# Optimization experiments

Hardware: AMD Instinct MI355X
Metric: run time of the kernel (lower is better)

Reference implementation:

```python
import jax, jax.numpy as jnp
import numpy as np

EARTH_R_MILES = 3958.8
NEG_INF = -1e30  # finite sentinel; exp underflows to 0 exactly

def haversine(lat1, lon1, lat2, lon2):
    lat1, lon1 = jnp.deg2rad(lat1), jnp.deg2rad(lon1)
    lat2, lon2 = jnp.deg2rad(lat2), jnp.deg2rad(lon2)
    dlat = lat2 - lat1
    dlon = lon2 - lon1
    a = jnp.sin(dlat / 2) ** 2 + jnp.cos(lat1) * jnp.cos(lat2) * jnp.sin(dlon / 2) ** 2
    c = 2.0 * jnp.arctan2(jnp.sqrt(a), jnp.sqrt(1.0 - a))
    return EARTH_R_MILES * c

def setup_inputs() -> dict:
    key = jax.random.key(0)
    k1, k2, k3, k4 = jax.random.split(key, 4)
    B, NBINS, M = 8192, 125, 4096
    preds_lonlat = jax.random.normal(k1, (B, 2), dtype=jnp.float32) * 10.0
    # candidate [lon, lat] coords per bin, padded to M
    bin_coords = jax.random.uniform(k2, (NBINS, M, 2), dtype=jnp.float32) * 10.0
    # three categorical columns, each in [0, 5)
    x_vals = jax.random.randint(k3, (B, 3), 0, 5, dtype=jnp.int64)
    # ragged bin sizes in [1, M] (non-empty; original skips empty bins)
    bin_counts = jax.random.randint(k4, (NBINS,), 1, M + 1, dtype=jnp.int64)
    return {"preds_lonlat": preds_lonlat, "bin_coords": bin_coords,
            "x_vals": x_vals, "bin_counts": bin_counts}

def reference(preds_lonlat, bin_coords, x_vals, bin_counts):
    tau = 0.25
    M = bin_coords.shape[1]
    # flat bin id from categorical key (5 categories per column)
    bin_ids = x_vals[:, 0] * 25 + x_vals[:, 1] * 5 + x_vals[:, 2]      # [B]
    cand = bin_coords[bin_ids]                                          # [B, M, 2] (lon, lat)
    counts = bin_counts[bin_ids]                                        # [B]
    mask = jnp.arange(M)[None, :] < counts[:, None]                     # [B, M]
    lon_p = preds_lonlat[:, 0:1]                                        # [B, 1]
    lat_p = preds_lonlat[:, 1:2]
    dists = haversine(lat_p, lon_p, cand[..., 1], cand[..., 0])         # [B, M]
    logits = jnp.where(mask, -dists / tau, NEG_INF)
    soft_min = -tau * jax.scipy.special.logsumexp(logits, axis=1)       # [B]
    valid = counts > 0
    n_valid = jnp.maximum(jnp.sum(valid), 1)
    loss = jnp.sum(jnp.where(valid, soft_min, 0.0)) / n_valid
    return loss
```

## Files before the change

### kernel.cpp

```cpp
#include <hip/hip_runtime.h>
#include <math.h>

#define D2R      0.017453292519943295f
#define TWO_R    7917.6f
#define RPI2     12435.698f
#define TAU_LN2  0.17328679513998632f
#define K_EXP2   5.770780163555854f
#define MBIG     1.0e30f
#define DMASK    2.0e30f
#define NBINS    125
#define P        8
#define CH       1024
#define MAXCH    4
#define NG_MAX   1152

__device__ __forceinline__ float fexp2(float x) { return __builtin_amdgcn_exp2f(x); }
__device__ __forceinline__ float rfl(float x) {
  return __int_as_float(__builtin_amdgcn_readfirstlane(__float_as_int(x)));
}

#define W_ACCF(w)   ((float*)(w))
#define W_ACCI(w)   ((int*)((char*)(w) + 4))
#define W_NG(w)     ((int*)((char*)(w) + 8))
#define W_HIST(w)   ((int*)((char*)(w) + 16))
#define W_CUR(w)    ((int*)((char*)(w) + 528))
#define W_PBASE(w)  ((int*)((char*)(w) + 1040))
#define W_WREC(w)   ((int4*)((char*)(w) + 1552))
#define W_PTRIG(w)  ((float4*)((char*)(w) + 19984))
#define W_PM(w)     ((float*)((char*)(w) + 151056))
#define W_PS(w)     ((float*)((char*)(w) + 298512))

__global__ __launch_bounds__(256) void g1_hist(
    const int* __restrict__ xv, void* __restrict__ w, int B) {
  int i = blockIdx.x * 256 + threadIdx.x;
  if (i < B) {
    int bin = xv[3 * i] * 25 + xv[3 * i + 1] * 5 + xv[3 * i + 2];
    atomicAdd(&W_HIST(w)[bin], 1);
  }
}

__global__ __launch_bounds__(128) void g2_scan(
    const int* __restrict__ bin_counts, void* __restrict__ w) {
  __shared__ int h[NBINS], cc[NBINS], pb[NBINS], gb[NBINS];
  const int t = threadIdx.x;
  if (t < NBINS) { h[t] = W_HIST(w)[t]; cc[t] = bin_counts[t]; }
  __syncthreads();
  if (t == 0) {
    int base = 0, g = 0;
    for (int b = 0; b < NBINS; ++b) {
      pb[b] = base; base += h[b];
      gb[b] = g;    g += (h[b] + P - 1) / P;
    }
    *W_NG(w) = g;
  }
  __syncthreads();
  if (t < NBINS) {
    W_PBASE(w)[t] = pb[t];
    int ng = (h[t] + P - 1) / P, g0 = gb[t], cnt = cc[t];
    for (int g = 0; g < ng; ++g) {
      int pbp = (pb[t] + g * P) | (min(P, h[t] - g * P) << 20);
      W_WREC(w)[g0 + g] = make_int4(t, pbp, cnt, g);
    }
  }
}

__global__ __launch_bounds__(256) void g3_scatter(
    const float2* __restrict__ preds, const int* __restrict__ xv,
    void* __restrict__ w, int B) {
  int i = blockIdx.x * 256 + threadIdx.x;
  if (i < B) {
    int bin = xv[3 * i] * 25 + xv[3 * i + 1] * 5 + xv[3 * i + 2];
    int pos = W_PBASE(w)[bin] + atomicAdd(&W_CUR(w)[bin], 1);
    float2 p = preds[i];
    float sA, cA, sO, cO;
    __sincosf(p.y * D2R, &sA, &cA);
    __sincosf(p.x * D2R, &sO, &cO);
    W_PTRIG(w)[pos] = make_float4(cA, sA, cO, sO);
  }
}

__global__ __launch_bounds__(256) void lse_main(
    const float2* __restrict__ bc, void* __restrict__ w, int M) {
  const int gi = blockIdx.x >> 2;
  if (gi >= *W_NG(w)) return;
  const int c = blockIdx.x & 3;

  const int4 rec = W_WREC(w)[gi];
  const int bin = rec.x, cnt = rec.z;
  const int nch = (cnt + CH - 1) >> 10;
  if (c >= nch) return;
  const int pb = rec.y & 0xFFFFF;
  const int tid = threadIdx.x;

  const float4* __restrict__ ptrig = W_PTRIG(w);
  const int pcm1 = (rec.y >> 20) - 1;
  float cA[P], sA[P], cO[P], sO[P];
#pragma unroll
  for (int p = 0; p < P; ++p) {
    float4 t = ptrig[pb + min(p, pcm1)];
    cA[p] = rfl(t.x); sA[p] = rfl(t.y); cO[p] = rfl(t.z); sO[p] = rfl(t.w);
  }

  const float2* __restrict__ cb = bc + (size_t)bin * (size_t)M;
  const int c0 = c << 10;
  const int cend = min(cnt, c0 + CH);
  const int nst = (cend - c0 + 255) >> 8;

  float m[P], s[P];
#pragma unroll
  for (int p = 0; p < P; ++p) { m[p] = MBIG; s[p] = 0.0f; }

  float2 cur = cb[min(c0 + tid, cend - 1)];
  for (int st = 0; st < nst; ++st) {
    const int idx = c0 + (st << 8) + tid;
    float2 nxt = cb[min(idx + 256, cend - 1)];
    float sla, cla, slo, clo;
    __sincosf(cur.y * D2R, &sla, &cla);
    __sincosf(cur.x * D2R, &slo, &clo);
    const bool valid = idx < cend;
#pragma unroll
    for (int p = 0; p < P; ++p) {
      float pp    = cA[p] * cla;
      float cdlat = fmaf(sA[p], sla, pp);
      float cdlon = fmaf(cO[p], clo, sO[p] * slo);
      float t1 = fmaf(-0.5f, cdlat, 0.5f);
      float t2 = fmaf(-0.5f, cdlon, 0.5f);
      float a  = fminf(fmaxf(fmaf(pp, t2, t1), 0.0f), 1.0f);
      float x  = sqrtf(a);
      float pl = fmaf(x, -0.0012624911f, 0.0066700901f);
      pl = fmaf(x, pl, -0.0170881256f);
      pl = fmaf(x, pl,  0.0308918810f);
      pl = fmaf(x, pl, -0.0501743046f);
      pl = fmaf(x, pl,  0.0889789874f);
      pl = fmaf(x, pl, -0.2145988016f);
      pl = fmaf(x, pl,  1.5707963050f);
      float wq = sqrtf(1.0f - x);
      float d  = fmaf(-TWO_R, wq * pl, RPI2);
      d = valid ? d : DMASK;
      float mn = fminf(m[p], d);
      s[p] = fmaf(s[p], fexp2((mn - m[p]) * K_EXP2), fexp2((mn - d) * K_EXP2));
      m[p] = mn;
    }
    cur = nxt;
  }

#pragma unroll
  for (int p = 0; p < P; ++p) {
    float mw = m[p];
#pragma unroll
    for (int o = 32; o; o >>= 1) mw = fminf(mw, __shfl_xor(mw, o));
    float sp = s[p] * fexp2((mw - m[p]) * K_EXP2);
#pragma unroll
    for (int o = 32; o; o >>= 1) sp += __shfl_xor(sp, o);
    m[p] = mw; s[p] = sp;
  }

  __shared__ float redm[4][P], reds[4][P];
  const int wave = tid >> 6;
  if ((tid & 63) == 0) {
#pragma unroll
    for (int p = 0; p < P; ++p) { redm[wave][p] = m[p]; reds[wave][p] = s[p]; }
  }
  __syncthreads();
  if (tid < P) {
    float M4 = fminf(fminf(redm[0][tid], redm[1][tid]),
                     fminf(redm[2][tid], redm[3][tid]));
    float S4 = reds[0][tid] * fexp2((M4 - redm[0][tid]) * K_EXP2)
             + reds[1][tid] * fexp2((M4 - redm[1][tid]) * K_EXP2)
             + reds[2][tid] * fexp2((M4 - redm[2][tid]) * K_EXP2)
             + reds[3][tid] * fexp2((M4 - redm[3][tid]) * K_EXP2);
    W_PM(w)[gi * 32 + (c << 3) + tid] = M4;
    W_PS(w)[gi * 32 + (c << 3) + tid] = S4;
  }
}

__global__ __launch_bounds__(64) void merge_kernel(void* __restrict__ w) {
  const int gi = blockIdx.x;
  if (gi >= *W_NG(w)) return;
  const int4 rec = W_WREC(w)[gi];
  const int cnt = rec.z;
  if (cnt <= 0) return;
  const int nch = (cnt + CH - 1) >> 10;
  const int pcount = rec.y >> 20;
  const int p = threadIdx.x;

  float soft = 0.0f;
  if (p < P) {
    float m = W_PM(w)[gi * 32 + p];
    float s = W_PS(w)[gi * 32 + p];
    for (int c = 1; c < nch; ++c) {
      float mo = W_PM(w)[gi * 32 + (c << 3) + p];
      float so = W_PS(w)[gi * 32 + (c << 3) + p];
      float mn = fminf(m, mo);
      s = fmaf(s, fexp2((mn - m) * K_EXP2), so * fexp2((mn - mo) * K_EXP2));
      m = mn;
    }
    float val = m - TAU_LN2 * __log2f(s);
    soft = (p < pcount) ? val : 0.0f;
  }
#pragma unroll
  for (int o = 32; o; o >>= 1) soft += __shfl_xor(soft, o);
  if (p == 0) {
    atomicAdd(W_ACCF(w), soft);
    atomicAdd(W_ACCI(w), pcount);
  }
}

__global__ void fin_kernel(const void* __restrict__ w, float* __restrict__ out) {
  int nv = *W_ACCI((void*)w);
  if (nv < 1) nv = 1;
  out[0] = *W_ACCF((void*)w) / (float)nv;
}

extern "C" void kernel_launch(void* const* d_in, const int* in_sizes, int n_in,
                              void* d_out, int out_size, void* d_ws, size_t ws_size,
                              hipStream_t stream) {
  const float2* preds      = (const float2*)d_in[0];
  const float2* bin_coords = (const float2*)d_in[1];
  const int*    x_vals     = (const int*)d_in[2];
  const int*    bin_counts = (const int*)d_in[3];
  float*        out        = (float*)d_out;

  const int B = in_sizes[0] / 2;
  const int M = (in_sizes[1] / 2) / NBINS;

  hipMemsetAsync(d_ws, 0, 1040, stream);

  const int pblk = (B + 255) / 256;
  g1_hist<<<pblk, 256, 0, stream>>>(x_vals, d_ws, B);
  g2_scan<<<1, 128, 0, stream>>>(bin_counts, d_ws);
  g3_scatter<<<pblk, 256, 0, stream>>>(preds, x_vals, d_ws, B);

  lse_main<<<NG_MAX * MAXCH, 256, 0, stream>>>(bin_coords, d_ws, M);

  merge_kernel<<<NG_MAX, 64, 0, stream>>>(d_ws);
  fin_kernel<<<1, 1, 0, stream>>>(d_ws, out);
}
```

Baseline: 167.9 us.

## Fuse grouping into one block and merge work into persistent main kernel

```diff
diff --git a/kernel.cpp b/kernel.cpp
--- a/kernel.cpp
+++ b/kernel.cpp
@@ -2,75 +2,76 @@
 #include <math.h>
 
 #define D2R      0.017453292519943295f
-#define TWO_R    7917.6f
-#define RPI2     12435.698f
 #define TAU_LN2  0.17328679513998632f
-#define K_EXP2   5.770780163555854f
+#define KR       45690.73f
+#define KRP      71763.68f
 #define MBIG     1.0e30f
 #define DMASK    2.0e30f
 #define NBINS    125
 #define P        8
 #define CH       1024
-#define MAXCH    4
 #define NG_MAX   1152
+#define NBLK     1024
 
 __device__ __forceinline__ float fexp2(float x) { return __builtin_amdgcn_exp2f(x); }
 __device__ __forceinline__ float rfl(float x) {
   return __int_as_float(__builtin_amdgcn_readfirstlane(__float_as_int(x)));
 }
 
-#define W_ACCF(w)   ((float*)(w))
-#define W_ACCI(w)   ((int*)((char*)(w) + 4))
-#define W_NG(w)     ((int*)((char*)(w) + 8))
-#define W_HIST(w)   ((int*)((char*)(w) + 16))
-#define W_CUR(w)    ((int*)((char*)(w) + 528))
-#define W_PBASE(w)  ((int*)((char*)(w) + 1040))
-#define W_WREC(w)   ((int4*)((char*)(w) + 1552))
-#define W_PTRIG(w)  ((float4*)((char*)(w) + 19984))
-#define W_PM(w)     ((float*)((char*)(w) + 151056))
-#define W_PS(w)     ((float*)((char*)(w) + 298512))
-
-__global__ __launch_bounds__(256) void g1_hist(
-    const int* __restrict__ xv, void* __restrict__ w, int B) {
-  int i = blockIdx.x * 256 + threadIdx.x;
-  if (i < B) {
+#define W_NI(w)    ((int*)(w))
+#define W_NGR(w)   ((int*)((char*)(w) + 4))
+#define W_DONE(w)  ((int*)((char*)(w) + 8))
+#define W_GREC(w)  ((int2*)((char*)(w) + 16))
+#define W_IREC(w)  ((int4*)((char*)(w) + 9232))
+#define W_PTRIG(w) ((float4*)((char*)(w) + 82960))
+#define W_PM(w)    ((float*)((char*)(w) + 214032))
+#define W_PS(w)    ((float*)((char*)(w) + 361488))
+
+__global__ __launch_bounds__(1024) void group_kernel(
+    const float2* __restrict__ preds, const int* __restrict__ xv,
+    const int* __restrict__ bin_counts, void* __restrict__ w, int B) {
+  __shared__ int h[NBINS], cur[NBINS], pb[NBINS], gb[NBINS], ib[NBINS], cc[NBINS];
+  const int tid = threadIdx.x;
+
+  if (tid < NBINS) { h[tid] = 0; cc[tid] = bin_counts[tid]; }
+  __syncthreads();
+
+  for (int i = tid; i < B; i += 1024) {
     int bin = xv[3 * i] * 25 + xv[3 * i + 1] * 5 + xv[3 * i + 2];
-    atomicAdd(&W_HIST(w)[bin], 1);
-  }
-}
-
-__global__ __launch_bounds__(128) void g2_scan(
-    const int* __restrict__ bin_counts, void* __restrict__ w) {
-  __shared__ int h[NBINS], cc[NBINS], pb[NBINS], gb[NBINS];
-  const int t = threadIdx.x;
-  if (t < NBINS) { h[t] = W_HIST(w)[t]; cc[t] = bin_counts[t]; }
-  __syncthreads();
-  if (t == 0) {
-    int base = 0, g = 0;
+    atomicAdd(&h[bin], 1);
+  }
+  __syncthreads();
+
+  if (tid == 0) {
+    int base = 0, g = 0, it = 0;
     for (int b = 0; b < NBINS; ++b) {
-      pb[b] = base; base += h[b];
-      gb[b] = g;    g += (h[b] + P - 1) / P;
-    }
-    *W_NG(w) = g;
-  }
-  __syncthreads();
-  if (t < NBINS) {
-    W_PBASE(w)[t] = pb[t];
-    int ng = (h[t] + P - 1) / P, g0 = gb[t], cnt = cc[t];
+      pb[b] = base; gb[b] = g; ib[b] = it;
+      int ngb  = (h[b] + 7) >> 3;
+      int nchb = (cc[b] + CH - 1) >> 10;
+      base += h[b]; g += ngb; it += ngb * nchb;
+    }
+    *W_NI(w) = it; *W_NGR(w) = g; *W_DONE(w) = 0;
+  }
+  __syncthreads();
+
+  if (tid < NBINS) {
+    cur[tid] = 0;
+    const int b = tid, hb = h[b], cb_ = cc[b];
+    const int ng = (hb + 7) >> 3, nch = (cb_ + CH - 1) >> 10;
+    const int g0 = gb[b], i0 = ib[b], p0 = pb[b];
     for (int g = 0; g < ng; ++g) {
-      int pbp = (pb[t] + g * P) | (min(P, h[t] - g * P) << 20);
-      W_WREC(w)[g0 + g] = make_int4(t, pbp, cnt, g);
-    }
-  }
-}
-
-__global__ __launch_bounds__(256) void g3_scatter(
-    const float2* __restrict__ preds, const int* __restrict__ xv,
-    void* __restrict__ w, int B) {
-  int i = blockIdx.x * 256 + threadIdx.x;
-  if (i < B) {
+      int pc = min(P, hb - g * P);
+      W_GREC(w)[g0 + g] = make_int2(pc, cb_);
+      for (int c = 0; c < nch; ++c)
+        W_IREC(w)[i0 + g * nch + c] =
+            make_int4(b, (p0 + g * P) | (pc << 20), cb_, ((g0 + g) << 2) | c);
+    }
+  }
+  __syncthreads();
+
+  for (int i = tid; i < B; i += 1024) {
     int bin = xv[3 * i] * 25 + xv[3 * i + 1] * 5 + xv[3 * i + 2];
-    int pos = W_PBASE(w)[bin] + atomicAdd(&W_CUR(w)[bin], 1);
+    int pos = pb[bin] + atomicAdd(&cur[bin], 1);
     float2 p = preds[i];
     float sA, cA, sO, cO;
     __sincosf(p.y * D2R, &sA, &cA);
@@ -79,137 +80,145 @@
   }
 }
 
-__global__ __launch_bounds__(256) void lse_main(
-    const float2* __restrict__ bc, void* __restrict__ w, int M) {
-  const int gi = blockIdx.x >> 2;
-  if (gi >= *W_NG(w)) return;
-  const int c = blockIdx.x & 3;
-
-  const int4 rec = W_WREC(w)[gi];
-  const int bin = rec.x, cnt = rec.z;
-  const int nch = (cnt + CH - 1) >> 10;
-  if (c >= nch) return;
-  const int pb = rec.y & 0xFFFFF;
-  const int tid = threadIdx.x;
-
-  const float4* __restrict__ ptrig = W_PTRIG(w);
-  const int pcm1 = (rec.y >> 20) - 1;
-  float cA[P], sA[P], cO[P], sO[P];
-#pragma unroll
-  for (int p = 0; p < P; ++p) {
-    float4 t = ptrig[pb + min(p, pcm1)];
-    cA[p] = rfl(t.x); sA[p] = rfl(t.y); cO[p] = rfl(t.z); sO[p] = rfl(t.w);
-  }
-
-  const float2* __restrict__ cb = bc + (size_t)bin * (size_t)M;
-  const int c0 = c << 10;
-  const int cend = min(cnt, c0 + CH);
-  const int nst = (cend - c0 + 255) >> 8;
-
-  float m[P], s[P];
-#pragma unroll
-  for (int p = 0; p < P; ++p) { m[p] = MBIG; s[p] = 0.0f; }
-
-  float2 cur = cb[min(c0 + tid, cend - 1)];
-  for (int st = 0; st < nst; ++st) {
-    const int idx = c0 + (st << 8) + tid;
-    float2 nxt = cb[min(idx + 256, cend - 1)];
-    float sla, cla, slo, clo;
-    __sincosf(cur.y * D2R, &sla, &cla);
-    __sincosf(cur.x * D2R, &slo, &clo);
-    const bool valid = idx < cend;
+__global__ __launch_bounds__(256) void main_kernel(
+    const float2* __restrict__ bc, void* __restrict__ w, int M,
+    float* __restrict__ out) {
+  const int bid = blockIdx.x, tid = threadIdx.x;
+  const int ni = *W_NI(w);
+
+  __shared__ float redm[4][P], reds[4][P];
+  __shared__ int sticket;
+
+  for (int i = bid; i < ni; i += NBLK) {
+    const int4 rec = W_IREC(w)[i];
+    const int bin = rec.x, cnt = rec.z;
+    const int pbb = rec.y & 0xFFFFF, pq = rec.y >> 20;
+    const int gi = rec.w >> 2, c = rec.w & 3;
+
+    float cA[P], sA[P], cO[P], sO[P];
 #pragma unroll
     for (int p = 0; p < P; ++p) {
-      float pp    = cA[p] * cla;
-      float cdlat = fmaf(sA[p], sla, pp);
-      float cdlon = fmaf(cO[p], clo, sO[p] * slo);
-      float t1 = fmaf(-0.5f, cdlat, 0.5f);
-      float t2 = fmaf(-0.5f, cdlon, 0.5f);
-      float a  = fminf(fmaxf(fmaf(pp, t2, t1), 0.0f), 1.0f);
-      float x  = sqrtf(a);
-      float pl = fmaf(x, -0.0012624911f, 0.0066700901f);
-      pl = fmaf(x, pl, -0.0170881256f);
-      pl = fmaf(x, pl,  0.0308918810f);
-      pl = fmaf(x, pl, -0.0501743046f);
-      pl = fmaf(x, pl,  0.0889789874f);
-      pl = fmaf(x, pl, -0.2145988016f);
-      pl = fmaf(x, pl,  1.5707963050f);
-      float wq = sqrtf(1.0f - x);
-      float d  = fmaf(-TWO_R, wq * pl, RPI2);
-      d = valid ? d : DMASK;
-      float mn = fminf(m[p], d);
-      s[p] = fmaf(s[p], fexp2((mn - m[p]) * K_EXP2), fexp2((mn - d) * K_EXP2));
-      m[p] = mn;
-    }
-    cur = nxt;
-  }
-
-#pragma unroll
-  for (int p = 0; p < P; ++p) {
-    float mw = m[p];
-#pragma unroll
-    for (int o = 32; o; o >>= 1) mw = fminf(mw, __shfl_xor(mw, o));
-    float sp = s[p] * fexp2((mw - m[p]) * K_EXP2);
-#pragma unroll
-    for (int o = 32; o; o >>= 1) sp += __shfl_xor(sp, o);
-    m[p] = mw; s[p] = sp;
-  }
-
-  __shared__ float redm[4][P], reds[4][P];
-  const int wave = tid >> 6;
-  if ((tid & 63) == 0) {
-#pragma unroll
-    for (int p = 0; p < P; ++p) { redm[wave][p] = m[p]; reds[wave][p] = s[p]; }
-  }
-  __syncthreads();
-  if (tid < P) {
-    float M4 = fminf(fminf(redm[0][tid], redm[1][tid]),
-                     fminf(redm[2][tid], redm[3][tid]));
-    float S4 = reds[0][tid] * fexp2((M4 - redm[0][tid]) * K_EXP2)
-             + reds[1][tid] * fexp2((M4 - redm[1][tid]) * K_EXP2)
-             + reds[2][tid] * fexp2((M4 - redm[2][tid]) * K_EXP2)
-             + reds[3][tid] * fexp2((M4 - redm[3][tid]) * K_EXP2);
-    W_PM(w)[gi * 32 + (c << 3) + tid] = M4;
-    W_PS(w)[gi * 32 + (c << 3) + tid] = S4;
-  }
-}
-
-__global__ __launch_bounds__(64) void merge_kernel(void* __restrict__ w) {
-  const int gi = blockIdx.x;
-  if (gi >= *W_NG(w)) return;
-  const int4 rec = W_WREC(w)[gi];
-  const int cnt = rec.z;
-  if (cnt <= 0) return;
-  const int nch = (cnt + CH - 1) >> 10;
-  const int pcount = rec.y >> 20;
-  const int p = threadIdx.x;
-
-  float soft = 0.0f;
-  if (p < P) {
-    float m = W_PM(w)[gi * 32 + p];
-    float s = W_PS(w)[gi * 32 + p];
-    for (int c = 1; c < nch; ++c) {
-      float mo = W_PM(w)[gi * 32 + (c << 3) + p];
-      float so = W_PS(w)[gi * 32 + (c << 3) + p];
-      float mn = fminf(m, mo);
-      s = fmaf(s, fexp2((mn - m) * K_EXP2), so * fexp2((mn - mo) * K_EXP2));
-      m = mn;
-    }
-    float val = m - TAU_LN2 * __log2f(s);
-    soft = (p < pcount) ? val : 0.0f;
-  }
-#pragma unroll
-  for (int o = 32; o; o >>= 1) soft += __shfl_xor(soft, o);
-  if (p == 0) {
-    atomicAdd(W_ACCF(w), soft);
-    atomicAdd(W_ACCI(w), pcount);
-  }
-}
-
-__global__ void fin_kernel(const void* __restrict__ w, float* __restrict__ out) {
-  int nv = *W_ACCI((void*)w);
-  if (nv < 1) nv = 1;
-  out[0] = *W_ACCF((void*)w) / (float)nv;
+      float4 t = W_PTRIG(w)[pbb + min(p, pq - 1)];
+      cA[p] = rfl(t.x); sA[p] = rfl(t.y); cO[p] = rfl(t.z); sO[p] = rfl(t.w);
+    }
+
+    const float2* __restrict__ cbp = bc + (size_t)bin * (size_t)M;
+    const int c0 = c << 10;
+    const int cend = min(cnt, c0 + CH);
+    const int nst = (cend - c0 + 255) >> 8;
+
+    float m[P], s[P];
+#pragma unroll
+    for (int p = 0; p < P; ++p) { m[p] = MBIG; s[p] = 0.0f; }
+
+    float2 curc = cbp[min(c0 + tid, cend - 1)];
+    for (int st = 0; st < nst; ++st) {
+      const int idx = c0 + (st << 8) + tid;
+      float2 nxt = cbp[min(idx + 256, cend - 1)];
+      float sla, cla, slo, clo;
+      __sincosf(curc.y * D2R, &sla, &cla);
+      __sincosf(curc.x * D2R, &slo, &clo);
+      const float nh_sla = -0.5f * sla, h_cla = 0.5f * cla;
+      const bool valid = idx < cend;
+#pragma unroll
+      for (int p = 0; p < P; ++p) {
+        float cdlon = fmaf(cO[p], clo, sO[p] * slo);
+        float a = fmaf(-(cA[p] * h_cla), cdlon, fmaf(sA[p], nh_sla, 0.5f));
+        a = fminf(fmaxf(a, 0.0f), 1.0f);
+        float x = sqrtf(a);
+        float pl = fmaf(x, -0.0012624911f, 0.0066700901f);
+        pl = fmaf(x, pl, -0.0170881256f);
+        pl = fmaf(x, pl,  0.0308918810f);
+        pl = fmaf(x, pl, -0.0501743046f);
+        pl = fmaf(x, pl,  0.0889789874f);
+        pl = fmaf(x, pl, -0.2145988016f);
+        pl = fmaf(x, pl,  1.5707963050f);
+        float wq = sqrtf(1.0f - x);
+        float dz = fmaf(-KR, wq * pl, KRP);
+        dz = valid ? dz : DMASK;
+        float mn = fminf(m[p], dz);
+        s[p] = fmaf(s[p], fexp2(mn - m[p]), fexp2(mn - dz));
+        m[p] = mn;
+      }
+      curc = nxt;
+    }
+
+#pragma unroll
+    for (int p = 0; p < P; ++p) {
+      float mw = m[p];
+#pragma unroll
+      for (int o = 32; o; o >>= 1) mw = fminf(mw, __shfl_xor(mw, o));
+      float sp = s[p] * fexp2(mw - m[p]);
+#pragma unroll
+      for (int o = 32; o; o >>= 1) sp += __shfl_xor(sp, o);
+      m[p] = mw; s[p] = sp;
+    }
+
+    const int wave = tid >> 6;
+    if ((tid & 63) == 0) {
+#pragma unroll
+      for (int p = 0; p < P; ++p) { redm[wave][p] = m[p]; reds[wave][p] = s[p]; }
+    }
+    __syncthreads();
+    if (tid < P) {
+      float M4 = fminf(fminf(redm[0][tid], redm[1][tid]),
+                       fminf(redm[2][tid], redm[3][tid]));
+      float S4 = reds[0][tid] * fexp2(M4 - redm[0][tid])
+               + reds[1][tid] * fexp2(M4 - redm[1][tid])
+               + reds[2][tid] * fexp2(M4 - redm[2][tid])
+               + reds[3][tid] * fexp2(M4 - redm[3][tid]);
+      W_PM(w)[gi * 32 + (c << 3) + tid] = M4;
+      W_PS(w)[gi * 32 + (c << 3) + tid] = S4;
+    }
+    __syncthreads();
+  }
+
+  if (tid == 0) {
+    __threadfence();
+    sticket = __hip_atomic_fetch_add(W_DONE(w), 1, __ATOMIC_ACQ_REL,
+                                     __HIP_MEMORY_SCOPE_AGENT);
+  }
+  __syncthreads();
+
+  if (sticket == NBLK - 1) {
+    const int ng = *W_NGR(w);
+    float accf = 0.0f; int accn = 0;
+    for (int t = tid; t < ng * P; t += 256) {
+      const int gi = t >> 3, p = t & 7;
+      const int2 gr = W_GREC(w)[gi];
+      const int pc = gr.x, cnt = gr.y;
+      if (cnt > 0) {
+        const int nch = (cnt + CH - 1) >> 10;
+        float mz = W_PM(w)[gi * 32 + p];
+        float sz = W_PS(w)[gi * 32 + p];
+        for (int c = 1; c < nch; ++c) {
+          float mo = W_PM(w)[gi * 32 + (c << 3) + p];
+          float so = W_PS(w)[gi * 32 + (c << 3) + p];
+          float mn = fminf(mz, mo);
+          sz = fmaf(sz, fexp2(mn - mz), so * fexp2(mn - mo));
+          mz = mn;
+        }
+        if (p < pc) accf += TAU_LN2 * (mz - __log2f(sz));
+        if (p == 0) accn += pc;
+      }
+    }
+#pragma unroll
+    for (int o = 32; o; o >>= 1) {
+      accf += __shfl_xor(accf, o);
+      accn += __shfl_xor(accn, o);
+    }
+    __shared__ float mf[4];
+    __shared__ int   mi[4];
+    const int wave = tid >> 6;
+    if ((tid & 63) == 0) { mf[wave] = accf; mi[wave] = accn; }
+    __syncthreads();
+    if (tid == 0) {
+      float f = mf[0] + mf[1] + mf[2] + mf[3];
+      int   n = mi[0] + mi[1] + mi[2] + mi[3];
+      if (n < 1) n = 1;
+      out[0] = f / (float)n;
+    }
+  }
 }
 
 extern "C" void kernel_launch(void* const* d_in, const int* in_sizes, int n_in,
@@ -224,15 +233,6 @@
   const int B = in_sizes[0] / 2;
   const int M = (in_sizes[1] / 2) / NBINS;
 
-  hipMemsetAsync(d_ws, 0, 1040, stream);
-
-  const int pblk = (B + 255) / 256;
-  g1_hist<<<pblk, 256, 0, stream>>>(x_vals, d_ws, B);
-  g2_scan<<<1, 128, 0, stream>>>(bin_counts, d_ws);
-  g3_scatter<<<pblk, 256, 0, stream>>>(preds, x_vals, d_ws, B);
-
-  lse_main<<<NG_MAX * MAXCH, 256, 0, stream>>>(bin_coords, d_ws, M);
-
-  merge_kernel<<<NG_MAX, 64, 0, stream>>>(d_ws);
-  fin_kernel<<<1, 1, 0, stream>>>(d_ws, out);
-}
+  group_kernel<<<1, 1024, 0, stream>>>(preds, x_vals, bin_counts, d_ws, B);
+  main_kernel<<<NBLK, 256, 0, stream>>>(bin_coords, d_ws, M, out);
+}
```

Result: no change. 169.5 us (+0.9%).
